# Kernel optimization log

Hardware: AMD Instinct MI355X
Metric: run time of the kernel (lower is better)

The kernel has to match this reference:

```python
import jax, jax.numpy as jnp
import numpy as np

EPS = 1e-5

def _conv(x, w, pad):
    # NCHW / OIHW 2-D convolution, stride 1
    return jax.lax.conv_general_dilated(
        x, w, window_strides=(1, 1), padding=[(pad, pad), (pad, pad)],
        dimension_numbers=('NCHW', 'OIHW', 'NCHW'))

def _bn2d(x, g, b, m, v):
    inv = g * jax.lax.rsqrt(v + EPS)
    return x * inv[None, :, None, None] + (b - m * inv)[None, :, None, None]

def _bn1d(x, g, b, m, v):
    inv = g * jax.lax.rsqrt(v + EPS)
    return x * inv[None, :] + (b - m * inv)[None, :]

def _avgpool2(x):
    B, C, H, W = x.shape
    return x.reshape(B, C, H // 2, 2, W // 2, 2).mean(axis=(3, 5))

def _hardtanh01(x):
    return jnp.clip(x, 0.0, 1.0)

def setup_inputs() -> dict:
    key = jax.random.key(0)
    ks = jax.random.split(key, 24)
    B = 1024
    d = {}
    d['x_in'] = jax.random.normal(ks[0], (B, 3, 32, 32), dtype=jnp.float32)
    d['w1'] = jax.random.normal(ks[1], (32, 3, 5, 5), dtype=jnp.float32) * 0.1
    d['w2'] = jax.random.normal(ks[2], (32, 32, 5, 5), dtype=jnp.float32) * 0.05
    d['w3'] = jax.random.normal(ks[3], (64, 32, 5, 5), dtype=jnp.float32) * 0.05
    d['w4'] = jax.random.normal(ks[4], (10, 64, 4, 4), dtype=jnp.float32) * 0.05
    for i, (c, k0) in enumerate([(32, 5), (32, 9), (64, 13), (10, 17)], start=1):
        d[f'g{i}'] = jax.random.uniform(ks[k0], (c,), minval=0.5, maxval=1.5, dtype=jnp.float32)
        d[f'b{i}'] = jax.random.normal(ks[k0 + 1], (c,), dtype=jnp.float32) * 0.1
        d[f'm{i}'] = jax.random.normal(ks[k0 + 2], (c,), dtype=jnp.float32) * 0.1
        d[f'v{i}'] = jax.random.uniform(ks[k0 + 3], (c,), minval=0.5, maxval=1.5, dtype=jnp.float32)
    return d

def reference(x_in, w1, w2, w3, w4,
              g1, b1, m1, v1, g2, b2, m2, v2,
              g3, b3, m3, v3, g4, b4, m4, v4):
    # conv1 -> bn1 -> pool -> hardtanh(0,1)
    x = _hardtanh01(_avgpool2(_bn2d(_conv(x_in, w1, 2), g1, b1, m1, v1)))
    # conv2 -> bn2 -> pool -> hardtanh(0,1)
    x = _hardtanh01(_avgpool2(_bn2d(_conv(x, w2, 2), g2, b2, m2, v2)))
    # conv3 -> bn3 -> pool -> hardtanh(0,1)
    x = _hardtanh01(_avgpool2(_bn2d(_conv(x, w3, 2), g3, b3, m3, v3)))
    # fc1 as 4x4 conv, valid padding -> (B, num_classes, 1, 1)
    x = _conv(x, w4, 0).reshape(x.shape[0], -1)
    return _bn1d(x, g4, b4, m4, v4)
```

## Files before the change

kernel.cpp:

```cpp
#include <hip/hip_runtime.h>

#define EPSF 1e-5f

typedef _Float16 half8 __attribute__((ext_vector_type(8)));
typedef _Float16 half4v __attribute__((ext_vector_type(4)));
typedef float f32x4 __attribute__((ext_vector_type(4)));

__device__ __forceinline__ float clamp01(float x){ return fminf(fmaxf(x, 0.f), 1.f); }

__global__ __launch_bounds__(256) void k_prep(
    const float* __restrict__ w1, const float* __restrict__ w2,
    const float* __restrict__ w3, const float* __restrict__ w4,
    const float* __restrict__ g1, const float* __restrict__ b1, const float* __restrict__ m1, const float* __restrict__ v1,
    const float* __restrict__ g2, const float* __restrict__ b2, const float* __restrict__ m2, const float* __restrict__ v2,
    const float* __restrict__ g3, const float* __restrict__ b3, const float* __restrict__ m3, const float* __restrict__ v3,
    const float* __restrict__ g4, const float* __restrict__ b4, const float* __restrict__ m4, const float* __restrict__ v4,
    _Float16* __restrict__ w1h, _Float16* __restrict__ w2h, _Float16* __restrict__ w3h,
    _Float16* __restrict__ w4h, float* __restrict__ bnc)
{
  const int t = blockIdx.x*256 + threadIdx.x;
  if (t < 5120) {
    int c = t / 160, k = t - c*160;
    int oc = (c < 16) ? 2*c : 2*(c-16)+1;
    int dy = k >> 5, rem = k & 31, dx = rem >> 2, ic = rem & 3;
    float val = (dx < 5 && ic < 3) ? w1[(oc*3+ic)*25 + dy*5 + dx] : 0.f;
    w1h[t] = (_Float16)val;
  }
  for (int i = t; i < 25600; i += 32768) {
    int tap = i >> 10, r = i & 1023, c = r >> 5, ic = r & 31;
    int oc = (c < 16) ? 2*c : 2*(c-16)+1;
    w2h[i] = (_Float16)w2[(oc*32+ic)*25 + tap];
  }
  for (int i = t; i < 51200; i += 32768) {
    int tap = i >> 11, r = i & 2047, oc = r >> 5, ic = r & 31;
    w3h[i] = (_Float16)w3[(oc*32+ic)*25 + tap];
  }
  for (int i = t; i < 16384; i += 32768) {
    int oc = i >> 10, k = i & 1023, pos = k >> 6, ic = k & 63;
    float val = (oc < 10) ? w4[(oc*64+ic)*16 + pos] : 0.f;
    w4h[i] = (_Float16)val;
  }
  if (t < 32) {
    float inv = g1[t] / sqrtf(v1[t] + EPSF);
    bnc[t] = 0.25f*inv; bnc[32+t] = b1[t] - m1[t]*inv;
    float i2 = g2[t] / sqrtf(v2[t] + EPSF);
    bnc[64+t] = 0.25f*i2; bnc[96+t] = b2[t] - m2[t]*i2;
  }
  if (t < 64) {
    float i3 = g3[t] / sqrtf(v3[t] + EPSF);
    bnc[128+t] = 0.25f*i3; bnc[192+t] = b3[t] - m3[t]*i3;
  }
  if (t < 10) {
    float i4 = g4[t] / sqrtf(v4[t] + EPSF);
    bnc[256+t] = i4; bnc[266+t] = b4[t] - m4[t]*i4;
  }
}

__global__ __launch_bounds__(512, 6) void k_fused(
    const float* __restrict__ x,
    const _Float16* __restrict__ w1h, const _Float16* __restrict__ w2h,
    const _Float16* __restrict__ w3h, const _Float16* __restrict__ w4h,
    const float* __restrict__ bnc, float* __restrict__ out)
{
  __shared__ __align__(16) char arena[32000];
  _Float16* Bx1 = (_Float16*)arena;
  float*    Img = (float*)(arena + 11264);
  _Float16* P2  = (_Float16*)arena;
  _Float16* P3  = (_Float16*)arena;
  _Float16* Ip3 = (_Float16*)(arena + 11520);
  float*    S4P = (float*)(arena + 13568);

  const int img = blockIdx.x;
  const int tid = threadIdx.x;
  const int w   = __builtin_amdgcn_readfirstlane(tid >> 6);
  const int l   = tid & 63;
  const int row = l & 15;
  const int kg  = l >> 4;
  const int mtb = w & 3;
  const int ntb = w >> 2;

  {
    const float4* src = (const float4*)(x + img*3072);
    float4* dst = (float4*)Img;
    dst[tid] = src[tid];
    if (tid < 256) dst[tid + 512] = src[tid + 512];
  }
  __syncthreads();

  for (int j = tid; j < 1400; j += 512) {
    int y = j / 40, xx = j - y*40;
    float s0 = 0.f, s1 = 0.f, s2 = 0.f;
    #pragma unroll
    for (int r = 0; r < 2; ++r) {
      int iy = y - 2 + r;
      if ((unsigned)iy < 32u) {
        #pragma unroll
        for (int cc = 0; cc < 2; ++cc) {
          int ix = xx - 2 + cc;
          if ((unsigned)ix < 32u) {
            const float* ip = Img + iy*32 + ix;
            s0 += ip[0]; s1 += ip[1024]; s2 += ip[2048];
          }
        }
      }
    }
    half4v h; h[0] = (_Float16)s0; h[1] = (_Float16)s1; h[2] = (_Float16)s2; h[3] = (_Float16)0.f;
    *(half4v*)(Bx1 + y*160 + xx*4) = h;
  }
  __syncthreads();

  f32x4 acc1[4];
  {
    half8 B1[5];
    #pragma unroll
    for (int dy = 0; dy < 5; ++dy)
      B1[dy] = *(const half8*)(w1h + (ntb*16 + row)*160 + dy*32 + kg*8);
    #pragma unroll
    for (int mt = 0; mt < 4; ++mt) acc1[mt] = (f32x4){0,0,0,0};
    const int xoff = 8*(row + kg);
    #pragma unroll
    for (int mt = 0; mt < 4; ++mt) {
      const int py = mtb*4 + mt;
      #pragma unroll
      for (int dy = 0; dy < 5; ++dy) {
        half8 av = *(const half8*)(Bx1 + (2*py + dy)*160 + xoff);
        acc1[mt] = __builtin_amdgcn_mfma_f32_16x16x32_f16(av, B1[dy], acc1[mt], 0, 0, 0);
      }
    }
  }
  __syncthreads();

  for (int j = tid; j < 1600; j += 512) {
    int u = j & 3, pos = j >> 2;
    int a = pos/20, c = pos - a*20;
    bool interior = ((unsigned)(a-2) < 16u) & ((unsigned)(c-2) < 16u);
    if (!interior) *(half8*)(P2 + pos*40 + u*8) = (half8)(_Float16)0.f;
  }
  {
    const int oc = 2*row + ntb;
    const float sA = bnc[oc], hA = bnc[32 + oc];
    #pragma unroll
    for (int mt = 0; mt < 4; ++mt) {
      const int py = mtb*4 + mt;
      #pragma unroll
      for (int r = 0; r < 4; ++r) {
        int pcol = kg*4 + r;
        int idx = ((py+2)*20 + pcol+2)*40;
        P2[idx + oc] = (_Float16)clamp01(fmaf(acc1[mt][r], sA, hA));
      }
    }
  }
  __syncthreads();

  f32x4 a2 = {0,0,0,0};
  {
    const int pixel = mtb*16 + row;
    const int py = pixel >> 3, px = pixel & 7;
    const _Float16* base = P2 + ((2*py)*20 + 2*px)*40 + kg*8;
    half8 RA[6], RB[6];
    #pragma unroll
    for (int c = 0; c < 6; ++c) RA[c] = *(const half8*)(base + c*40);
    #pragma unroll
    for (int c = 0; c < 6; ++c) RB[c] = *(const half8*)(base + 800 + c*40);
    const _Float16* wb = w2h + (ntb*16 + row)*32 + kg*8;
    half8 cw = *(const half8*)(wb);
    #pragma unroll
    for (int dy = 0; dy < 5; ++dy) {
      half8 cs[6];
      #pragma unroll
      for (int c = 0; c < 6; ++c) cs[c] = RA[c] + RB[c];
      if (dy < 4) {
        #pragma unroll
        for (int c = 0; c < 6; ++c) {
          half8 nv = *(const half8*)(base + (dy+2)*800 + c*40);
          if ((dy & 1) == 0) RA[c] = nv; else RB[c] = nv;
        }
      }
      #pragma unroll
      for (int dx = 0; dx < 5; ++dx) {
        const int tap = dy*5 + dx;
        const int tn = (tap < 24) ? tap + 1 : 24;
        half8 nw = *(const half8*)(wb + tn*1024);
        half8 av = cs[dx] + cs[dx+1];
        a2 = __builtin_amdgcn_mfma_f32_16x16x32_f16(av, cw, a2, 0, 0, 0);
        cw = nw;
      }
    }
  }
  __syncthreads();

  for (int j = tid; j < 576; j += 512) {
    int u = j & 3, pos = j >> 2;
    int a = pos/12, c = pos - a*12;
    bool interior = ((unsigned)(a-2) < 8u) & ((unsigned)(c-2) < 8u);
    if (!interior) *(half8*)(P3 + pos*40 + u*8) = (half8)(_Float16)0.f;
  }
  {
    const int oc = 2*row + ntb;
    const float sA = bnc[64 + oc], hA = bnc[96 + oc];
    #pragma unroll
    for (int r = 0; r < 4; ++r) {
      int p2 = mtb*16 + kg*4 + r;
      int py2 = p2 >> 3, px2 = p2 & 7;
      int idx = ((py2+2)*12 + px2+2)*40;
      P3[idx + oc] = (_Float16)clamp01(fmaf(a2[r], sA, hA));
    }
  }
  __syncthreads();

  if (w < 4) {
    const int py = row >> 2, px = row & 3;
    const _Float16* base = P3 + ((2*py)*12 + 2*px)*40 + kg*8;
    half8 RA[6], RB[6];
    #pragma unroll
    for (int c = 0; c < 6; ++c) RA[c] = *(const half8*)(base + c*40);
    #pragma unroll
    for (int c = 0; c < 6; ++c) RB[c] = *(const half8*)(base + 480 + c*40);
    const _Float16* wb = w3h + (w*16 + row)*32 + kg*8;
    half8 cw = *(const half8*)(wb);
    f32x4 a3 = {0,0,0,0};
    #pragma unroll
    for (int dy = 0; dy < 5; ++dy) {
      half8 cs[6];
      #pragma unroll
      for (int c = 0; c < 6; ++c) cs[c] = RA[c] + RB[c];
      if (dy < 4) {
        #pragma unroll
        for (int c = 0; c < 6; ++c) {
          half8 nv = *(const half8*)(base + (dy+2)*480 + c*40);
          if ((dy & 1) == 0) RA[c] = nv; else RB[c] = nv;
        }
      }
      #pragma unroll
      for (int dx = 0; dx < 5; ++dx) {
        const int tap = dy*5 + dx;
        const int tn = (tap < 24) ? tap + 1 : 24;
        half8 nw = *(const half8*)(wb + tn*2048);
        half8 av = cs[dx] + cs[dx+1];
        a3 = __builtin_amdgcn_mfma_f32_16x16x32_f16(av, cw, a3, 0, 0, 0);
        cw = nw;
      }
    }
    const int oc = w*16 + row;
    const float s3 = bnc[128 + oc], h3 = bnc[192 + oc];
    #pragma unroll
    for (int r = 0; r < 4; ++r)
      Ip3[(kg*4 + r)*64 + oc] = (_Float16)clamp01(fmaf(a3[r], s3, h3));
  }
  __syncthreads();

  if (tid < 160) {
    const int oc = tid >> 4, pix = tid & 15;
    const _Float16* A = Ip3 + pix*64;
    const _Float16* W = w4h + oc*1024 + pix*64;
    float a = 0.f;
    #pragma unroll
    for (int q = 0; q < 8; ++q) {
      half8 xa = *(const half8*)(A + q*8);
      half8 wv = *(const half8*)(W + q*8);
      #pragma unroll
      for (int j = 0; j < 8; ++j)
        a = fmaf((float)xa[j], (float)wv[j], a);
    }
    S4P[tid] = a;
  }
  __syncthreads();
  if (tid < 10) {
    float s = 0.f;
    #pragma unroll
    for (int i = 0; i < 16; ++i) s += S4P[tid*16 + i];
    out[img*10 + tid] = fmaf(s, bnc[256 + tid], bnc[266 + tid]);
  }
}

extern "C" void kernel_launch(void* const* d_in, const int* in_sizes, int n_in,
                              void* d_out, int out_size, void* d_ws, size_t ws_size,
                              hipStream_t stream)
{
  const float* x  = (const float*)d_in[0];
  const float* w1 = (const float*)d_in[1];
  const float* w2 = (const float*)d_in[2];
  const float* w3 = (const float*)d_in[3];
  const float* w4 = (const float*)d_in[4];
  const float *g1=(const float*)d_in[5],  *b1=(const float*)d_in[6],
              *m1=(const float*)d_in[7],  *v1=(const float*)d_in[8];
  const float *g2=(const float*)d_in[9],  *b2=(const float*)d_in[10],
              *m2=(const float*)d_in[11], *v2=(const float*)d_in[12];
  const float *g3=(const float*)d_in[13], *b3=(const float*)d_in[14],
              *m3=(const float*)d_in[15], *v3=(const float*)d_in[16];
  const float *g4=(const float*)d_in[17], *b4=(const float*)d_in[18],
              *m4=(const float*)d_in[19], *v4=(const float*)d_in[20];
  float* out = (float*)d_out;

  char* ws = (char*)d_ws;
  _Float16* w1h = (_Float16*)(ws);
  _Float16* w2h = (_Float16*)(ws + 10240);
  _Float16* w3h = (_Float16*)(ws + 61440);
  _Float16* w4h = (_Float16*)(ws + 163840);
  float*    bnc = (float*)   (ws + 196608);

  k_prep<<<dim3(128), dim3(256), 0, stream>>>(w1, w2, w3, w4,
      g1,b1,m1,v1, g2,b2,m2,v2, g3,b3,m3,v3, g4,b4,m4,v4,
      w1h, w2h, w3h, w4h, bnc);
  k_fused<<<dim3(1024), dim3(512), 0, stream>>>(x, w1h, w2h, w3h, w4h, bnc, out);
}
```

Before: 129.8 us.

## Fold 2x2 avg-pool box filter into effective 6x6 conv weights

Before, each conv layer built pooled sums of activations at runtime: a 2x2 box-summed input image for conv1 and in-register half8 adds for conv2 and conv3. Now the 2x2 box filter is folded into the weights in the prep kernel, giving 6x6 effective kernels evaluated as strided convolutions. This removes the activation box-sum adds and the float image staging, and the input now goes straight into a padded fp16 layout. The cost is 36 MFMA taps instead of 25 per layer, more weight traffic, and an extra zeroing pass over shared memory.

```diff
diff --git a/kernel.cpp b/kernel.cpp
--- a/kernel.cpp
+++ b/kernel.cpp
@@ -3,7 +3,6 @@
 #define EPSF 1e-5f
 
 typedef _Float16 half8 __attribute__((ext_vector_type(8)));
-typedef _Float16 half4v __attribute__((ext_vector_type(4)));
 typedef float f32x4 __attribute__((ext_vector_type(4)));
 
 __device__ __forceinline__ float clamp01(float x){ return fminf(fmaxf(x, 0.f), 1.f); }
@@ -15,25 +14,55 @@
     const float* __restrict__ g2, const float* __restrict__ b2, const float* __restrict__ m2, const float* __restrict__ v2,
     const float* __restrict__ g3, const float* __restrict__ b3, const float* __restrict__ m3, const float* __restrict__ v3,
     const float* __restrict__ g4, const float* __restrict__ b4, const float* __restrict__ m4, const float* __restrict__ v4,
-    _Float16* __restrict__ w1h, _Float16* __restrict__ w2h, _Float16* __restrict__ w3h,
+    _Float16* __restrict__ w1e, _Float16* __restrict__ w2e, _Float16* __restrict__ w3e,
     _Float16* __restrict__ w4h, float* __restrict__ bnc)
 {
   const int t = blockIdx.x*256 + threadIdx.x;
-  if (t < 5120) {
-    int c = t / 160, k = t - c*160;
+  if (t < 6144) {
+    int c = t / 192, k = t - c*192;
     int oc = (c < 16) ? 2*c : 2*(c-16)+1;
-    int dy = k >> 5, rem = k & 31, dx = rem >> 2, ic = rem & 3;
-    float val = (dx < 5 && ic < 3) ? w1[(oc*3+ic)*25 + dy*5 + dx] : 0.f;
-    w1h[t] = (_Float16)val;
-  }
-  for (int i = t; i < 25600; i += 32768) {
-    int tap = i >> 10, r = i & 1023, c = r >> 5, ic = r & 31;
+    int u = k >> 5, rem = k & 31, v = rem >> 2, ic = rem & 3;
+    float val = 0.f;
+    if (v < 6 && ic < 3) {
+      #pragma unroll
+      for (int r = 0; r < 2; ++r)
+        #pragma unroll
+        for (int cc = 0; cc < 2; ++cc) {
+          int uu = u - r, vv = v - cc;
+          if ((unsigned)uu < 5u && (unsigned)vv < 5u)
+            val += w1[(oc*3+ic)*25 + uu*5 + vv];
+        }
+    }
+    w1e[t] = (_Float16)val;
+  }
+  for (int i = t; i < 36864; i += 32768) {
+    int tap = i >> 10, r2 = i & 1023, c = r2 >> 5, ic = r2 & 31;
     int oc = (c < 16) ? 2*c : 2*(c-16)+1;
-    w2h[i] = (_Float16)w2[(oc*32+ic)*25 + tap];
-  }
-  for (int i = t; i < 51200; i += 32768) {
-    int tap = i >> 11, r = i & 2047, oc = r >> 5, ic = r & 31;
-    w3h[i] = (_Float16)w3[(oc*32+ic)*25 + tap];
+    int u = tap / 6, v = tap - u*6;
+    float val = 0.f;
+    #pragma unroll
+    for (int r = 0; r < 2; ++r)
+      #pragma unroll
+      for (int cc = 0; cc < 2; ++cc) {
+        int uu = u - r, vv = v - cc;
+        if ((unsigned)uu < 5u && (unsigned)vv < 5u)
+          val += w2[(oc*32+ic)*25 + uu*5 + vv];
+      }
+    w2e[i] = (_Float16)val;
+  }
+  for (int i = t; i < 73728; i += 32768) {
+    int tap = i >> 11, r2 = i & 2047, oc = r2 >> 5, ic = r2 & 31;
+    int u = tap / 6, v = tap - u*6;
+    float val = 0.f;
+    #pragma unroll
+    for (int r = 0; r < 2; ++r)
+      #pragma unroll
+      for (int cc = 0; cc < 2; ++cc) {
+        int uu = u - r, vv = v - cc;
+        if ((unsigned)uu < 5u && (unsigned)vv < 5u)
+          val += w3[(oc*32+ic)*25 + uu*5 + vv];
+      }
+    w3e[i] = (_Float16)val;
   }
   for (int i = t; i < 16384; i += 32768) {
     int oc = i >> 10, k = i & 1023, pos = k >> 6, ic = k & 63;
@@ -58,17 +87,16 @@
 
 __global__ __launch_bounds__(512, 6) void k_fused(
     const float* __restrict__ x,
-    const _Float16* __restrict__ w1h, const _Float16* __restrict__ w2h,
-    const _Float16* __restrict__ w3h, const _Float16* __restrict__ w4h,
+    const _Float16* __restrict__ w1e, const _Float16* __restrict__ w2e,
+    const _Float16* __restrict__ w3e, const _Float16* __restrict__ w4h,
     const float* __restrict__ bnc, float* __restrict__ out)
 {
   __shared__ __align__(16) char arena[32000];
-  _Float16* Bx1 = (_Float16*)arena;
-  float*    Img = (float*)(arena + 11264);
-  _Float16* P2  = (_Float16*)arena;
-  _Float16* P3  = (_Float16*)arena;
-  _Float16* Ip3 = (_Float16*)(arena + 11520);
-  float*    S4P = (float*)(arena + 13568);
+  _Float16* Pimg = (_Float16*)arena;
+  _Float16* P2   = (_Float16*)arena;
+  _Float16* P3   = (_Float16*)arena;
+  _Float16* Ip3  = (_Float16*)(arena + 11520);
+  float*    S4P  = (float*)(arena + 13568);
 
   const int img = blockIdx.x;
   const int tid = threadIdx.x;
@@ -79,52 +107,39 @@
   const int mtb = w & 3;
   const int ntb = w >> 2;
 
-  {
-    const float4* src = (const float4*)(x + img*3072);
-    float4* dst = (float4*)Img;
-    dst[tid] = src[tid];
-    if (tid < 256) dst[tid + 512] = src[tid + 512];
-  }
-  __syncthreads();
-
-  for (int j = tid; j < 1400; j += 512) {
-    int y = j / 40, xx = j - y*40;
-    float s0 = 0.f, s1 = 0.f, s2 = 0.f;
-    #pragma unroll
-    for (int r = 0; r < 2; ++r) {
-      int iy = y - 2 + r;
-      if ((unsigned)iy < 32u) {
-        #pragma unroll
-        for (int cc = 0; cc < 2; ++cc) {
-          int ix = xx - 2 + cc;
-          if ((unsigned)ix < 32u) {
-            const float* ip = Img + iy*32 + ix;
-            s0 += ip[0]; s1 += ip[1024]; s2 += ip[2048];
-          }
-        }
-      }
-    }
-    half4v h; h[0] = (_Float16)s0; h[1] = (_Float16)s1; h[2] = (_Float16)s2; h[3] = (_Float16)0.f;
-    *(half4v*)(Bx1 + y*160 + xx*4) = h;
+  for (int i = tid; i < 720; i += 512)
+    ((float4*)arena)[i] = make_float4(0.f,0.f,0.f,0.f);
+  __syncthreads();
+
+  {
+    const float* xin = x + img*3072;
+    for (int i = tid; i < 768; i += 512) {
+      int ic = i >> 8, rem = i & 255;
+      int y = rem >> 3, xq = rem & 7;
+      float4 v4 = *(const float4*)(xin + ic*1024 + y*32 + xq*4);
+      _Float16* dst = Pimg + (y+2)*160 + (xq*4 + 2)*4 + ic;
+      dst[0]  = (_Float16)v4.x; dst[4]  = (_Float16)v4.y;
+      dst[8]  = (_Float16)v4.z; dst[12] = (_Float16)v4.w;
+    }
   }
   __syncthreads();
 
   f32x4 acc1[4];
   {
-    half8 B1[5];
-    #pragma unroll
-    for (int dy = 0; dy < 5; ++dy)
-      B1[dy] = *(const half8*)(w1h + (ntb*16 + row)*160 + dy*32 + kg*8);
-    #pragma unroll
-    for (int mt = 0; mt < 4; ++mt) acc1[mt] = (f32x4){0,0,0,0};
+    half8 B1[6];
+    #pragma unroll
+    for (int u = 0; u < 6; ++u)
+      B1[u] = *(const half8*)(w1e + (ntb*16 + row)*192 + u*32 + kg*8);
+    #pragma unroll
+    for (int t2 = 0; t2 < 4; ++t2) acc1[t2] = (f32x4){0,0,0,0};
     const int xoff = 8*(row + kg);
     #pragma unroll
-    for (int mt = 0; mt < 4; ++mt) {
-      const int py = mtb*4 + mt;
-      #pragma unroll
-      for (int dy = 0; dy < 5; ++dy) {
-        half8 av = *(const half8*)(Bx1 + (2*py + dy)*160 + xoff);
-        acc1[mt] = __builtin_amdgcn_mfma_f32_16x16x32_f16(av, B1[dy], acc1[mt], 0, 0, 0);
+    for (int t2 = 0; t2 < 4; ++t2) {
+      const int py = mtb*4 + t2;
+      #pragma unroll
+      for (int u = 0; u < 6; ++u) {
+        half8 av = *(const half8*)(Pimg + (2*py + u)*160 + xoff);
+        acc1[t2] = __builtin_amdgcn_mfma_f32_16x16x32_f16(av, B1[u], acc1[t2], 0, 0, 0);
       }
     }
   }
@@ -140,13 +155,12 @@
     const int oc = 2*row + ntb;
     const float sA = bnc[oc], hA = bnc[32 + oc];
     #pragma unroll
-    for (int mt = 0; mt < 4; ++mt) {
-      const int py = mtb*4 + mt;
+    for (int t2 = 0; t2 < 4; ++t2) {
+      const int py = mtb*4 + t2;
       #pragma unroll
       for (int r = 0; r < 4; ++r) {
-        int pcol = kg*4 + r;
-        int idx = ((py+2)*20 + pcol+2)*40;
-        P2[idx + oc] = (_Float16)clamp01(fmaf(acc1[mt][r], sA, hA));
+        int px = kg*4 + r;
+        P2[((py+2)*20 + px+2)*40 + oc] = (_Float16)clamp01(fmaf(acc1[t2][r], sA, hA));
       }
     }
   }
@@ -156,36 +170,22 @@
   {
     const int pixel = mtb*16 + row;
     const int py = pixel >> 3, px = pixel & 7;
-    const _Float16* base = P2 + ((2*py)*20 + 2*px)*40 + kg*8;
-    half8 RA[6], RB[6];
-    #pragma unroll
-    for (int c = 0; c < 6; ++c) RA[c] = *(const half8*)(base + c*40);
-    #pragma unroll
-    for (int c = 0; c < 6; ++c) RB[c] = *(const half8*)(base + 800 + c*40);
-    const _Float16* wb = w2h + (ntb*16 + row)*32 + kg*8;
-    half8 cw = *(const half8*)(wb);
-    #pragma unroll
-    for (int dy = 0; dy < 5; ++dy) {
-      half8 cs[6];
-      #pragma unroll
-      for (int c = 0; c < 6; ++c) cs[c] = RA[c] + RB[c];
-      if (dy < 4) {
-        #pragma unroll
-        for (int c = 0; c < 6; ++c) {
-          half8 nv = *(const half8*)(base + (dy+2)*800 + c*40);
-          if ((dy & 1) == 0) RA[c] = nv; else RB[c] = nv;
-        }
-      }
-      #pragma unroll
-      for (int dx = 0; dx < 5; ++dx) {
-        const int tap = dy*5 + dx;
-        const int tn = (tap < 24) ? tap + 1 : 24;
+    const _Float16* base = P2 + (2*py)*800 + (2*px)*40 + kg*8;
+    const _Float16* wb = w2e + (ntb*16 + row)*32 + kg*8;
+    half8 wreg[4];
+    #pragma unroll
+    for (int q = 0; q < 4; ++q) wreg[q] = *(const half8*)(wb + q*1024);
+    #pragma unroll
+    for (int u = 0; u < 6; ++u)
+      #pragma unroll
+      for (int v = 0; v < 6; ++v) {
+        const int tap = u*6 + v;
+        const int tn = (tap < 32) ? tap + 4 : tap;
         half8 nw = *(const half8*)(wb + tn*1024);
-        half8 av = cs[dx] + cs[dx+1];
-        a2 = __builtin_amdgcn_mfma_f32_16x16x32_f16(av, cw, a2, 0, 0, 0);
-        cw = nw;
-      }
-    }
+        half8 av = *(const half8*)(base + u*800 + v*40);
+        a2 = __builtin_amdgcn_mfma_f32_16x16x32_f16(av, wreg[tap & 3], a2, 0, 0, 0);
+        wreg[tap & 3] = nw;
+      }
   }
   __syncthreads();
 
@@ -202,45 +202,30 @@
     for (int r = 0; r < 4; ++r) {
       int p2 = mtb*16 + kg*4 + r;
       int py2 = p2 >> 3, px2 = p2 & 7;
-      int idx = ((py2+2)*12 + px2+2)*40;
-      P3[idx + oc] = (_Float16)clamp01(fmaf(a2[r], sA, hA));
+      P3[((py2+2)*12 + px2+2)*40 + oc] = (_Float16)clamp01(fmaf(a2[r], sA, hA));
     }
   }
   __syncthreads();
 
   if (w < 4) {
     const int py = row >> 2, px = row & 3;
-    const _Float16* base = P3 + ((2*py)*12 + 2*px)*40 + kg*8;
-    half8 RA[6], RB[6];
-    #pragma unroll
-    for (int c = 0; c < 6; ++c) RA[c] = *(const half8*)(base + c*40);
-    #pragma unroll
-    for (int c = 0; c < 6; ++c) RB[c] = *(const half8*)(base + 480 + c*40);
-    const _Float16* wb = w3h + (w*16 + row)*32 + kg*8;
-    half8 cw = *(const half8*)(wb);
+    const _Float16* base = P3 + (2*py)*480 + (2*px)*40 + kg*8;
+    const _Float16* wb = w3e + (w*16 + row)*32 + kg*8;
+    half8 wreg[4];
+    #pragma unroll
+    for (int q = 0; q < 4; ++q) wreg[q] = *(const half8*)(wb + q*2048);
     f32x4 a3 = {0,0,0,0};
     #pragma unroll
-    for (int dy = 0; dy < 5; ++dy) {
-      half8 cs[6];
-      #pragma unroll
-      for (int c = 0; c < 6; ++c) cs[c] = RA[c] + RB[c];
-      if (dy < 4) {
-        #pragma unroll
-        for (int c = 0; c < 6; ++c) {
-          half8 nv = *(const half8*)(base + (dy+2)*480 + c*40);
-          if ((dy & 1) == 0) RA[c] = nv; else RB[c] = nv;
-        }
-      }
-      #pragma unroll
-      for (int dx = 0; dx < 5; ++dx) {
-        const int tap = dy*5 + dx;
-        const int tn = (tap < 24) ? tap + 1 : 24;
+    for (int u = 0; u < 6; ++u)
+      #pragma unroll
+      for (int v = 0; v < 6; ++v) {
+        const int tap = u*6 + v;
+        const int tn = (tap < 32) ? tap + 4 : tap;
         half8 nw = *(const half8*)(wb + tn*2048);
-        half8 av = cs[dx] + cs[dx+1];
-        a3 = __builtin_amdgcn_mfma_f32_16x16x32_f16(av, cw, a3, 0, 0, 0);
-        cw = nw;
-      }
-    }
+        half8 av = *(const half8*)(base + u*480 + v*40);
+        a3 = __builtin_amdgcn_mfma_f32_16x16x32_f16(av, wreg[tap & 3], a3, 0, 0, 0);
+        wreg[tap & 3] = nw;
+      }
     const int oc = w*16 + row;
     const float s3 = bnc[128 + oc], h3 = bnc[192 + oc];
     #pragma unroll
@@ -293,14 +278,14 @@
   float* out = (float*)d_out;
 
   char* ws = (char*)d_ws;
-  _Float16* w1h = (_Float16*)(ws);
-  _Float16* w2h = (_Float16*)(ws + 10240);
-  _Float16* w3h = (_Float16*)(ws + 61440);
-  _Float16* w4h = (_Float16*)(ws + 163840);
-  float*    bnc = (float*)   (ws + 196608);
+  _Float16* w1e = (_Float16*)(ws);
+  _Float16* w2e = (_Float16*)(ws + 12288);
+  _Float16* w3e = (_Float16*)(ws + 86016);
+  _Float16* w4h = (_Float16*)(ws + 233472);
+  float*    bnc = (float*)   (ws + 266240);
 
   k_prep<<<dim3(128), dim3(256), 0, stream>>>(w1, w2, w3, w4,
       g1,b1,m1,v1, g2,b2,m2,v2, g3,b3,m3,v3, g4,b4,m4,v4,
-      w1h, w2h, w3h, w4h, bnc);
-  k_fused<<<dim3(1024), dim3(512), 0, stream>>>(x, w1h, w2h, w3h, w4h, bnc, out);
+      w1e, w2e, w3e, w4h, bnc);
+  k_fused<<<dim3(1024), dim3(512), 0, stream>>>(x, w1e, w2e, w3e, w4h, bnc, out);
 }
```

Result: slower. 135.3 us (+4.2%).
